# Optimization experiments

Hardware: AMD Instinct MI355X
Metric: run time of the kernel (lower is better)

Reference implementation:

```python
import jax, jax.numpy as jnp
import numpy as np


def _cdist(x, y):
    # x: (b, n, c), y: (b, m, c) -> (b, n, m) Euclidean distances
    x2 = jnp.sum(x * x, axis=-1, keepdims=True)          # (b, n, 1)
    y2 = jnp.sum(y * y, axis=-1)[:, None, :]             # (b, 1, m)
    xy = jnp.einsum('bnc,bmc->bnm', x, y)                # (b, n, m)
    d2 = jnp.maximum(x2 + y2 - 2.0 * xy, 0.0)
    return jnp.sqrt(d2)


def setup_inputs() -> dict:
    key = jax.random.key(0)
    k1, k2, k3, k4 = jax.random.split(key, 4)
    bs, N, M, C = 8, 4096, 4096, 128
    return {
        'set1': jax.random.normal(k1, (bs, N, C), dtype=jnp.float32),
        'set2': jax.random.normal(k2, (bs, M, C), dtype=jnp.float32),
        'w1': jax.random.uniform(k3, (bs, N), dtype=jnp.float32),
        'w2': jax.random.uniform(k4, (bs, M), dtype=jnp.float32),
    }


def reference(set1, set2, w1, w2):
    dist = _cdist(set1, set2)                 # (b, N, M)
    out_dist = jnp.min(dist, axis=2)          # (b, N)
    out_dist2 = jnp.min(dist, axis=1)         # (b, M)
    total = (jnp.sum(w1 * out_dist) + jnp.sum(w2 * out_dist2)) / 2.0
    return total
```

## Files before the change

kernel.cpp:

```cpp
#include <hip/hip_runtime.h>

#define BS 8
#define NN 4096
#define MM 4096
#define CC 128
#define XT 128
#define YT 128
#define MH 2048
#define NMT (MH / YT)
#define NPH (2 * NMT)
#define NXT (NN / XT)
#define SLICE (YT * 64)

#define FINF_BITS 0x7F800000u

typedef __attribute__((ext_vector_type(8))) short bf16x8;
typedef __attribute__((ext_vector_type(4))) float f32x4;

#define WAITVn(n) asm volatile("s_waitcnt vmcnt(" #n ")" ::: "memory")
#define SCHED_FENCE() __builtin_amdgcn_sched_barrier(0)

__device__ inline ushort f2bf(float f) {
    unsigned u = __float_as_uint(f);
    unsigned r = (u + 0x7FFFu + ((u >> 16) & 1u)) >> 16;
    return (ushort)r;
}

__global__ void ch_prep(const float* __restrict__ y,
                        ushort* __restrict__ y16, float* __restrict__ yn,
                        unsigned* __restrict__ rowmin, unsigned* __restrict__ colmin,
                        float* __restrict__ out) {
    int gid = blockIdx.x * blockDim.x + threadIdx.x;
    size_t i = (size_t)gid * 8;

    float4 w0 = *(const float4*)(y + i);
    float4 w1 = *(const float4*)(y + i + 4);
    ushort h[8] = {f2bf(w0.x), f2bf(w0.y), f2bf(w0.z), f2bf(w0.w),
                   f2bf(w1.x), f2bf(w1.y), f2bf(w1.z), f2bf(w1.w)};
    *(bf16x8*)(y16 + i) = *(bf16x8*)h;
    float sy = w0.x * w0.x + w0.y * w0.y + w0.z * w0.z + w0.w * w0.w +
               w1.x * w1.x + w1.y * w1.y + w1.z * w1.z + w1.w * w1.w;

#pragma unroll
    for (int mask = 1; mask <= 8; mask <<= 1)
        sy += __shfl_xor(sy, mask, 64);
    if ((threadIdx.x & 15) == 0)
        yn[gid >> 4] = sy;

    if (gid < BS * NN) rowmin[gid] = FINF_BITS;
    if (gid < BS * MM) colmin[gid] = FINF_BITS;
    if (gid == 0) out[0] = 0.0f;
}

__device__ __forceinline__ void stage_y(const ushort* __restrict__ Yb,
                                        ushort* __restrict__ buf,
                                        int tile, int half, int tid, int wave) {
#pragma unroll
    for (int s = 0; s < 4; ++s) {
        int f = s * 256 + tid;
        int r = f >> 3, cslot = f & 7;
        const ushort* g = Yb + (size_t)(tile * YT + r) * CC + half * 64 +
                          ((cslot ^ (r & 7)) * 8);
        ushort* l = buf + (size_t)(s * 256 + wave * 64) * 8;
        __builtin_amdgcn_global_load_lds(
            (const __attribute__((address_space(1))) void*)g,
            (__attribute__((address_space(3))) void*)l, 16, 0, 0);
    }
}

__global__ __launch_bounds__(256, 2) void ch_tile(
    const float* __restrict__ Xf, const ushort* __restrict__ Y,
    const float* __restrict__ yn,
    unsigned* __restrict__ rowmin, unsigned* __restrict__ colmin) {

    __shared__ ushort pool[3 * SLICE];
    __shared__ unsigned coltile[MH];
    __shared__ unsigned rowtile[XT];
    __shared__ float xnorm[XT];
    __shared__ float ynld[MH];

    const int b  = blockIdx.x;
    const int xt = blockIdx.y;
    const int mh = blockIdx.z;
    const int n0 = xt * XT;
    const int m0 = mh * MH;
    const int tid  = threadIdx.x;
    const int lane = tid & 63;
    const int wave = tid >> 6;
    const int lc   = lane & 15;
    const int quad = lane >> 4;
    const int wm = wave >> 1;
    const int wn = wave & 1;

    const ushort* Yb = Y + ((size_t)b * MM + m0) * CC;

    ushort* xs = pool;
    const float* Xb = Xf + ((size_t)b * NN + n0) * CC;
    {
        float psum[8];
#pragma unroll
        for (int s = 0; s < 8; ++s) {
            int flat = s * 256 + tid;
            int r = flat >> 4, c = flat & 15;
            float4 v0 = *(const float4*)(Xb + (size_t)r * CC + c * 8);
            float4 v1 = *(const float4*)(Xb + (size_t)r * CC + c * 8 + 4);
            ushort h[8] = {f2bf(v0.x), f2bf(v0.y), f2bf(v0.z), f2bf(v0.w),
                           f2bf(v1.x), f2bf(v1.y), f2bf(v1.z), f2bf(v1.w)};
            *(bf16x8*)(xs + r * CC + (c ^ (r & 7)) * 8) = *(bf16x8*)h;
            psum[s] = v0.x * v0.x + v0.y * v0.y + v0.z * v0.z + v0.w * v0.w +
                      v1.x * v1.x + v1.y * v1.y + v1.z * v1.z + v1.w * v1.w;
        }
#pragma unroll
        for (int mask = 1; mask <= 8; mask <<= 1)
#pragma unroll
            for (int s = 0; s < 8; ++s)
                psum[s] += __shfl_xor(psum[s], mask, 64);
        if ((tid & 15) == 0) {
#pragma unroll
            for (int s = 0; s < 8; ++s)
                xnorm[s * 16 + (tid >> 4)] = psum[s];
        }
    }
    {
        const float* ynb = yn + (size_t)b * MM + m0;
#pragma unroll
        for (int s = 0; s < MH / 256; ++s)
            ynld[s * 256 + tid] = ynb[s * 256 + tid];
    }
    for (int c2 = tid; c2 < MH; c2 += 256) coltile[c2] = FINF_BITS;
    if (tid < XT) rowtile[tid] = FINF_BITS;

    __syncthreads();

    bf16x8 af[4][4];
    const int xrow = (wm * 64 + lc) * CC;
    const int xsw  = lc & 7;
#pragma unroll
    for (int kt = 0; kt < 4; ++kt)
#pragma unroll
        for (int i = 0; i < 4; ++i)
            af[kt][i] = *(const bf16x8*)(xs + xrow + i * 16 * CC +
                                         ((kt * 4 + quad) ^ xsw) * 8);

    float xnp[4][4];
#pragma unroll
    for (int i = 0; i < 4; ++i) {
        float4 t = *(const float4*)(&xnorm[wm * 64 + i * 16 + quad * 4]);
        xnp[i][0] = t.x; xnp[i][1] = t.y; xnp[i][2] = t.z; xnp[i][3] = t.w;
    }
    float rm[4][4];
#pragma unroll
    for (int i = 0; i < 4; ++i)
#pragma unroll
        for (int r = 0; r < 4; ++r) rm[i][r] = __builtin_inff();

    __syncthreads();

    stage_y(Yb, pool + 0 * SLICE, 0, 0, tid, wave);
    stage_y(Yb, pool + 1 * SLICE, 0, 1, tid, wave);
    WAITVn(4);
    __builtin_amdgcn_s_barrier();
    SCHED_FENCE();

    int rd = 0;
#pragma unroll 1
    for (int t = 0; t < NMT; ++t) {
        f32x4 acc[4][4];
        const f32x4 z = {0.f, 0.f, 0.f, 0.f};
        float ynr[4];

        {
            const int ph = 2 * t;
            const ushort* ybuf = pool + rd * SLICE;
            if (ph + 2 < NPH) {
                int wr = rd + 2; if (wr >= 3) wr -= 3;
                stage_y(Yb, pool + wr * SLICE, (ph + 2) >> 1, (ph + 2) & 1,
                        tid, wave);
            }
#pragma unroll
            for (int j = 0; j < 4; ++j)
                ynr[j] = ynld[t * YT + wn * 64 + j * 16 + lc];
#pragma unroll
            for (int s2 = 0; s2 < 2; ++s2) {
                bf16x8 yf[4];
                const int cy = ((s2 * 4 + quad) ^ xsw) * 8;
#pragma unroll
                for (int j = 0; j < 4; ++j)
                    yf[j] = *(const bf16x8*)(ybuf + (wn * 64 + j * 16 + lc) * 64 + cy);
                __builtin_amdgcn_s_setprio(1);
#pragma unroll
                for (int j = 0; j < 4; ++j)
#pragma unroll
                    for (int i = 0; i < 4; ++i)
                        acc[i][j] = __builtin_amdgcn_mfma_f32_16x16x32_bf16(
                            af[s2][i], yf[j], (s2 == 0) ? z : acc[i][j], 0, 0, 0);
                __builtin_amdgcn_s_setprio(0);
            }
            SCHED_FENCE();
            if (ph + 2 < NPH) { WAITVn(4); } else { WAITVn(0); }
            __builtin_amdgcn_s_barrier();
            SCHED_FENCE();
            rd = (rd == 2) ? 0 : rd + 1;
        }

        {
            const int ph = 2 * t + 1;
            const ushort* ybuf = pool + rd * SLICE;
            if (ph + 2 < NPH) {
                int wr = rd + 2; if (wr >= 3) wr -= 3;
                stage_y(Yb, pool + wr * SLICE, (ph + 2) >> 1, (ph + 2) & 1,
                        tid, wave);
            }
#pragma unroll
            for (int s2 = 0; s2 < 2; ++s2) {
                bf16x8 yf[4];
                const int cy = ((s2 * 4 + quad) ^ xsw) * 8;
#pragma unroll
                for (int j = 0; j < 4; ++j)
                    yf[j] = *(const bf16x8*)(ybuf + (wn * 64 + j * 16 + lc) * 64 + cy);
                __builtin_amdgcn_s_setprio(1);
#pragma unroll
                for (int j = 0; j < 4; ++j)
#pragma unroll
                    for (int i = 0; i < 4; ++i)
                        acc[i][j] = __builtin_amdgcn_mfma_f32_16x16x32_bf16(
                            af[2 + s2][i], yf[j], acc[i][j], 0, 0, 0);
                __builtin_amdgcn_s_setprio(0);
            }

            float cmv[4];
#pragma unroll
            for (int j = 0; j < 4; ++j) cmv[j] = __builtin_inff();
#pragma unroll
            for (int i = 0; i < 4; ++i) {
#pragma unroll
                for (int j = 0; j < 4; ++j) {
                    f32x4 a = acc[i][j];
                    float e[4];
#pragma unroll
                    for (int r = 0; r < 4; ++r)
                        e[r] = xnp[i][r] + fmaf(-2.0f, a[r], ynr[j]);
#pragma unroll
                    for (int r = 0; r < 4; ++r)
                        rm[i][r] = fminf(rm[i][r], e[r]);
                    cmv[j] = fminf(cmv[j],
                                   fminf(fminf(e[0], e[1]), fminf(e[2], e[3])));
                }
            }
#pragma unroll
            for (int mask = 16; mask <= 32; mask <<= 1)
#pragma unroll
                for (int j = 0; j < 4; ++j)
                    cmv[j] = fminf(cmv[j], __shfl_xor(cmv[j], mask, 64));
            if (quad == 0) {
#pragma unroll
                for (int j = 0; j < 4; ++j)
                    atomicMin(&coltile[t * YT + wn * 64 + j * 16 + lc],
                              __float_as_uint(fmaxf(cmv[j], 0.0f)));
            }

            SCHED_FENCE();
            if (ph + 2 < NPH) { WAITVn(4); } else { WAITVn(0); }
            __builtin_amdgcn_s_barrier();
            SCHED_FENCE();
            rd = (rd == 2) ? 0 : rd + 1;
        }
    }

#pragma unroll
    for (int mask = 1; mask <= 8; mask <<= 1)
#pragma unroll
        for (int i = 0; i < 4; ++i)
#pragma unroll
            for (int r = 0; r < 4; ++r)
                rm[i][r] = fminf(rm[i][r], __shfl_xor(rm[i][r], mask, 64));
    if (lc == 0) {
#pragma unroll
        for (int i = 0; i < 4; ++i)
#pragma unroll
            for (int r = 0; r < 4; ++r)
                atomicMin(&rowtile[wm * 64 + i * 16 + quad * 4 + r],
                          __float_as_uint(fmaxf(rm[i][r], 0.0f)));
    }

    __syncthreads();
    if (tid < XT)
        atomicMin(&rowmin[(size_t)b * NN + n0 + tid], rowtile[tid]);
    for (int c2 = tid; c2 < MH; c2 += 256)
        atomicMin(&colmin[(size_t)b * MM + m0 + c2], coltile[c2]);
}

__global__ void ch_finalize(const unsigned* __restrict__ rowmin,
                            const unsigned* __restrict__ colmin,
                            const float* __restrict__ w1,
                            const float* __restrict__ w2,
                            float* __restrict__ out) {
    int i = blockIdx.x * blockDim.x + threadIdx.x;
    int stride = gridDim.x * blockDim.x;
    float s = 0.f;
    for (int idx = i; idx < BS * NN; idx += stride)
        s += w1[idx] * sqrtf(__uint_as_float(rowmin[idx])) +
             w2[idx] * sqrtf(__uint_as_float(colmin[idx]));
#pragma unroll
    for (int off = 32; off > 0; off >>= 1) s += __shfl_down(s, off, 64);
    __shared__ float ls[4];
    int lane = threadIdx.x & 63, wv = threadIdx.x >> 6;
    if (lane == 0) ls[wv] = s;
    __syncthreads();
    if (threadIdx.x == 0) {
        float t = ls[0] + ls[1] + ls[2] + ls[3];
        atomicAdd(out, 0.5f * t);
    }
}

extern "C" void kernel_launch(void* const* d_in, const int* in_sizes, int n_in,
                              void* d_out, int out_size, void* d_ws, size_t ws_size,
                              hipStream_t stream) {
    const float* set1 = (const float*)d_in[0];
    const float* set2 = (const float*)d_in[1];
    const float* w1   = (const float*)d_in[2];
    const float* w2   = (const float*)d_in[3];
    float* out = (float*)d_out;

    ushort*   y16    = (ushort*)d_ws;
    float*    yn     = (float*)(y16 + (size_t)BS * MM * CC);
    unsigned* rowmin = (unsigned*)(yn + BS * MM);
    unsigned* colmin = rowmin + BS * NN;

    ch_prep<<<BS * MM * CC / 8 / 256, 256, 0, stream>>>(
        set2, y16, yn, rowmin, colmin, out);

    dim3 grid(BS, NXT, MM / MH);
    ch_tile<<<grid, 256, 0, stream>>>(set1, y16, yn, rowmin, colmin);

    ch_finalize<<<64, 256, 0, stream>>>(rowmin, colmin, w1, w2, out);
}
```

Measured before the change: 125.4 us.

## Switch distance GEMM from 16x16x32 to 32x32x16 bf16 MFMA tiles

Replaces the 4x4 grid of 16x16x32 MFMAs per wave with a 2x2 grid of 32x32x16 MFMAs, reorganizing A/B fragment loads, the x-norm layout and the row/column min epilogue to fit the 32x32 accumulator layout. Larger MFMA tiles need fewer instructions and fewer LDS fragment reads per FLOP, and the column-min reduction needs one fewer shuffle stage. The cost is a longer row-min shuffle reduction at the end, different register pressure from 16-wide accumulators, and removal of the s_setprio hints around the MFMA blocks.

```diff
diff --git a/kernel.cpp b/kernel.cpp
--- a/kernel.cpp
+++ b/kernel.cpp
@@ -15,7 +15,7 @@
 #define FINF_BITS 0x7F800000u
 
 typedef __attribute__((ext_vector_type(8))) short bf16x8;
-typedef __attribute__((ext_vector_type(4))) float f32x4;
+typedef __attribute__((ext_vector_type(16))) float f32x16;
 
 #define WAITVn(n) asm volatile("s_waitcnt vmcnt(" #n ")" ::: "memory")
 #define SCHED_FENCE() __builtin_amdgcn_sched_barrier(0)
@@ -87,8 +87,9 @@
     const int tid  = threadIdx.x;
     const int lane = tid & 63;
     const int wave = tid >> 6;
-    const int lc   = lane & 15;
-    const int quad = lane >> 4;
+    const int l31  = lane & 31;
+    const int hi   = lane >> 5;
+    const int lsw  = lane & 7;
     const int wm = wave >> 1;
     const int wn = wave & 1;
 
@@ -132,27 +133,28 @@
 
     __syncthreads();
 
-    bf16x8 af[4][4];
-    const int xrow = (wm * 64 + lc) * CC;
-    const int xsw  = lc & 7;
-#pragma unroll
-    for (int kt = 0; kt < 4; ++kt)
-#pragma unroll
-        for (int i = 0; i < 4; ++i)
-            af[kt][i] = *(const bf16x8*)(xs + xrow + i * 16 * CC +
-                                         ((kt * 4 + quad) ^ xsw) * 8);
-
-    float xnp[4][4];
-#pragma unroll
-    for (int i = 0; i < 4; ++i) {
-        float4 t = *(const float4*)(&xnorm[wm * 64 + i * 16 + quad * 4]);
-        xnp[i][0] = t.x; xnp[i][1] = t.y; xnp[i][2] = t.z; xnp[i][3] = t.w;
-    }
-    float rm[4][4];
-#pragma unroll
-    for (int i = 0; i < 4; ++i)
-#pragma unroll
-        for (int r = 0; r < 4; ++r) rm[i][r] = __builtin_inff();
+    bf16x8 af[8][2];
+#pragma unroll
+    for (int ks = 0; ks < 8; ++ks)
+#pragma unroll
+        for (int i = 0; i < 2; ++i) {
+            const int row = wm * 64 + i * 32 + l31;
+            af[ks][i] = *(const bf16x8*)(xs + row * CC +
+                                         ((ks * 2 + hi) ^ lsw) * 8);
+        }
+
+    float4 xnp[2][4];
+#pragma unroll
+    for (int i = 0; i < 2; ++i)
+#pragma unroll
+        for (int q = 0; q < 4; ++q)
+            xnp[i][q] = *(const float4*)(&xnorm[wm * 64 + i * 32 + q * 8 + 4 * hi]);
+
+    float rm[2][16];
+#pragma unroll
+    for (int i = 0; i < 2; ++i)
+#pragma unroll
+        for (int r = 0; r < 16; ++r) rm[i][r] = __builtin_inff();
 
     __syncthreads();
 
@@ -163,11 +165,13 @@
     SCHED_FENCE();
 
     int rd = 0;
+    const f32x16 z = {0.f, 0.f, 0.f, 0.f, 0.f, 0.f, 0.f, 0.f,
+                      0.f, 0.f, 0.f, 0.f, 0.f, 0.f, 0.f, 0.f};
+    f32x16 acc[2][2];
+
 #pragma unroll 1
     for (int t = 0; t < NMT; ++t) {
-        f32x4 acc[4][4];
-        const f32x4 z = {0.f, 0.f, 0.f, 0.f};
-        float ynr[4];
+        float ynr[2];
 
         {
             const int ph = 2 * t;
@@ -178,23 +182,24 @@
                         tid, wave);
             }
 #pragma unroll
-            for (int j = 0; j < 4; ++j)
-                ynr[j] = ynld[t * YT + wn * 64 + j * 16 + lc];
-#pragma unroll
-            for (int s2 = 0; s2 < 2; ++s2) {
-                bf16x8 yf[4];
-                const int cy = ((s2 * 4 + quad) ^ xsw) * 8;
-#pragma unroll
-                for (int j = 0; j < 4; ++j)
-                    yf[j] = *(const bf16x8*)(ybuf + (wn * 64 + j * 16 + lc) * 64 + cy);
-                __builtin_amdgcn_s_setprio(1);
-#pragma unroll
-                for (int j = 0; j < 4; ++j)
-#pragma unroll
-                    for (int i = 0; i < 4; ++i)
-                        acc[i][j] = __builtin_amdgcn_mfma_f32_16x16x32_bf16(
-                            af[s2][i], yf[j], (s2 == 0) ? z : acc[i][j], 0, 0, 0);
-                __builtin_amdgcn_s_setprio(0);
+            for (int j = 0; j < 2; ++j)
+                ynr[j] = ynld[t * YT + wn * 64 + j * 32 + l31];
+
+#pragma unroll
+            for (int ks = 0; ks < 4; ++ks) {
+                bf16x8 yf[2];
+#pragma unroll
+                for (int j = 0; j < 2; ++j) {
+                    const int row = wn * 64 + j * 32 + l31;
+                    yf[j] = *(const bf16x8*)(ybuf + row * 64 +
+                                             ((ks * 2 + hi) ^ lsw) * 8);
+                }
+#pragma unroll
+                for (int j = 0; j < 2; ++j)
+#pragma unroll
+                    for (int i = 0; i < 2; ++i)
+                        acc[i][j] = __builtin_amdgcn_mfma_f32_32x32x16_bf16(
+                            af[ks][i], yf[j], (ks == 0) ? z : acc[i][j], 0, 0, 0);
             }
             SCHED_FENCE();
             if (ph + 2 < NPH) { WAITVn(4); } else { WAITVn(0); }
@@ -212,50 +217,52 @@
                         tid, wave);
             }
 #pragma unroll
-            for (int s2 = 0; s2 < 2; ++s2) {
-                bf16x8 yf[4];
-                const int cy = ((s2 * 4 + quad) ^ xsw) * 8;
-#pragma unroll
-                for (int j = 0; j < 4; ++j)
-                    yf[j] = *(const bf16x8*)(ybuf + (wn * 64 + j * 16 + lc) * 64 + cy);
-                __builtin_amdgcn_s_setprio(1);
-#pragma unroll
-                for (int j = 0; j < 4; ++j)
-#pragma unroll
-                    for (int i = 0; i < 4; ++i)
-                        acc[i][j] = __builtin_amdgcn_mfma_f32_16x16x32_bf16(
-                            af[2 + s2][i], yf[j], acc[i][j], 0, 0, 0);
-                __builtin_amdgcn_s_setprio(0);
-            }
-
-            float cmv[4];
-#pragma unroll
-            for (int j = 0; j < 4; ++j) cmv[j] = __builtin_inff();
-#pragma unroll
-            for (int i = 0; i < 4; ++i) {
-#pragma unroll
-                for (int j = 0; j < 4; ++j) {
-                    f32x4 a = acc[i][j];
-                    float e[4];
-#pragma unroll
-                    for (int r = 0; r < 4; ++r)
-                        e[r] = xnp[i][r] + fmaf(-2.0f, a[r], ynr[j]);
-#pragma unroll
-                    for (int r = 0; r < 4; ++r)
-                        rm[i][r] = fminf(rm[i][r], e[r]);
-                    cmv[j] = fminf(cmv[j],
-                                   fminf(fminf(e[0], e[1]), fminf(e[2], e[3])));
+            for (int ks = 0; ks < 4; ++ks) {
+                bf16x8 yf[2];
+#pragma unroll
+                for (int j = 0; j < 2; ++j) {
+                    const int row = wn * 64 + j * 32 + l31;
+                    yf[j] = *(const bf16x8*)(ybuf + row * 64 +
+                                             ((ks * 2 + hi) ^ lsw) * 8);
                 }
-            }
-#pragma unroll
-            for (int mask = 16; mask <= 32; mask <<= 1)
-#pragma unroll
-                for (int j = 0; j < 4; ++j)
-                    cmv[j] = fminf(cmv[j], __shfl_xor(cmv[j], mask, 64));
-            if (quad == 0) {
-#pragma unroll
-                for (int j = 0; j < 4; ++j)
-                    atomicMin(&coltile[t * YT + wn * 64 + j * 16 + lc],
+#pragma unroll
+                for (int j = 0; j < 2; ++j)
+#pragma unroll
+                    for (int i = 0; i < 2; ++i)
+                        acc[i][j] = __builtin_amdgcn_mfma_f32_32x32x16_bf16(
+                            af[4 + ks][i], yf[j], acc[i][j], 0, 0, 0);
+            }
+
+            float cmv[2] = {__builtin_inff(), __builtin_inff()};
+#pragma unroll
+            for (int i = 0; i < 2; ++i) {
+#pragma unroll
+                for (int j = 0; j < 2; ++j) {
+                    f32x16 a = acc[i][j];
+                    float m = __builtin_inff();
+#pragma unroll
+                    for (int q = 0; q < 4; ++q) {
+                        float4 xq = xnp[i][q];
+                        float e0 = xq.x + fmaf(-2.0f, a[q * 4 + 0], ynr[j]);
+                        float e1 = xq.y + fmaf(-2.0f, a[q * 4 + 1], ynr[j]);
+                        float e2 = xq.z + fmaf(-2.0f, a[q * 4 + 2], ynr[j]);
+                        float e3 = xq.w + fmaf(-2.0f, a[q * 4 + 3], ynr[j]);
+                        rm[i][q * 4 + 0] = fminf(rm[i][q * 4 + 0], e0);
+                        rm[i][q * 4 + 1] = fminf(rm[i][q * 4 + 1], e1);
+                        rm[i][q * 4 + 2] = fminf(rm[i][q * 4 + 2], e2);
+                        rm[i][q * 4 + 3] = fminf(rm[i][q * 4 + 3], e3);
+                        m = fminf(m, fminf(fminf(e0, e1), fminf(e2, e3)));
+                    }
+                    cmv[j] = fminf(cmv[j], m);
+                }
+            }
+#pragma unroll
+            for (int j = 0; j < 2; ++j)
+                cmv[j] = fminf(cmv[j], __shfl_xor(cmv[j], 32, 64));
+            if (hi == 0) {
+#pragma unroll
+                for (int j = 0; j < 2; ++j)
+                    atomicMin(&coltile[t * YT + wn * 64 + j * 32 + l31],
                               __float_as_uint(fmaxf(cmv[j], 0.0f)));
             }
 
@@ -268,19 +275,21 @@
     }
 
 #pragma unroll
-    for (int mask = 1; mask <= 8; mask <<= 1)
-#pragma unroll
-        for (int i = 0; i < 4; ++i)
-#pragma unroll
-            for (int r = 0; r < 4; ++r)
+    for (int mask = 1; mask <= 16; mask <<= 1)
+#pragma unroll
+        for (int i = 0; i < 2; ++i)
+#pragma unroll
+            for (int r = 0; r < 16; ++r)
                 rm[i][r] = fminf(rm[i][r], __shfl_xor(rm[i][r], mask, 64));
-    if (lc == 0) {
-#pragma unroll
-        for (int i = 0; i < 4; ++i)
-#pragma unroll
-            for (int r = 0; r < 4; ++r)
-                atomicMin(&rowtile[wm * 64 + i * 16 + quad * 4 + r],
-                          __float_as_uint(fmaxf(rm[i][r], 0.0f)));
+    if (l31 == 0) {
+#pragma unroll
+        for (int i = 0; i < 2; ++i)
+#pragma unroll
+            for (int q = 0; q < 4; ++q)
+#pragma unroll
+                for (int c = 0; c < 4; ++c)
+                    atomicMin(&rowtile[wm * 64 + i * 32 + q * 8 + 4 * hi + c],
+                              __float_as_uint(fmaxf(rm[i][q * 4 + c], 0.0f)));
     }
 
     __syncthreads();
```

Result: no change. 126.9 us (+1.2%).
